# Performance work log

Measured on AMD Instinct MI355X. Metric: run time of the kernel, lower is better.

## Reference

```python
import jax, jax.numpy as jnp
import numpy as np

B, L, R, E, D = 16, 28, 64, 34, 512


def setup_inputs() -> dict:
    key = jax.random.key(0)
    ks = jax.random.split(key, 10)
    logits = jax.random.uniform(ks[0], (B, L, R), dtype=jnp.float32)
    evt_embeddings = jax.random.normal(ks[1], (B, 1, D), dtype=jnp.float32)
    arg_embeddings = jax.random.normal(ks[2], (B, L, D), dtype=jnp.float32)
    # valid-arg counts in [1, L] (used as mask-count multiplier and divisor)
    arg_padding_num = jax.random.randint(ks[3], (B,), 1, L + 1).astype(jnp.float32)
    evt_type_list = jax.random.randint(ks[4], (B,), 0, E)
    s = 1.0 / np.sqrt(D)
    WRT = jax.random.normal(ks[5], (R, D, D), dtype=jnp.float32) * s
    WTT = jax.random.normal(ks[6], (E, D, D), dtype=jnp.float32) * s
    w1 = jax.random.normal(ks[7], (D, 64), dtype=jnp.float32) * s
    b1 = jnp.zeros((64,), dtype=jnp.float32)
    w2 = jax.random.normal(ks[8], (64, 1), dtype=jnp.float32) * (1.0 / 8.0)
    b2 = jnp.zeros((1,), dtype=jnp.float32)
    return {"logits": logits, "evt_embeddings": evt_embeddings,
            "arg_embeddings": arg_embeddings, "arg_padding_num": arg_padding_num,
            "evt_type_list": evt_type_list, "WRT": WRT, "WTT": WTT,
            "w1": w1, "b1": b1, "w2": w2, "b2": b2}


def reference(logits, evt_embeddings, arg_embeddings, arg_padding_num,
              evt_type_list, WRT, WTT, w1, b1, w2, b2):
    # role transition matrix per (event, arg): one-hot/soft select over WRT
    # [B,L,R] x [R,D,D] -> [B,L,D,D]  (dominant, memory-bound intermediate)
    role_mats = jnp.einsum('blr,rde->blde', logits, WRT)
    # event transition matrix: one-hot select over WTT == gather
    evt_mats = WTT[evt_type_list]                      # [B,D,D]
    # event embedding transform: [B,1,D] bmm [B,D,D] -> [B,D]
    evt_trans = jnp.einsum('bd,bde->be', evt_embeddings[:, 0, :], evt_mats)
    # per-arg transform: [B,L,D] bmm [B,L,D,D] -> [B,L,D]
    role_trans = jnp.einsum('bld,blde->ble', arg_embeddings, role_mats)
    # multiply by count, sum over args, divide by count (as in the original)
    role_trans = role_trans * arg_padding_num[:, None, None]
    new_sum = jnp.sum(role_trans, axis=1)              # [B,D]
    div = new_sum / arg_padding_num[:, None]
    graph_embeddings = (div + evt_trans) / 2.0         # [B,D]
    # scorer MLP: Linear(D,64) -> ReLU -> Linear(64,1) -> Sigmoid
    h = jax.nn.relu(graph_embeddings @ w1 + b1)
    score = jax.nn.sigmoid(h @ w2 + b2)                # [B,1]
    return score
```

## Files before the change

kernel.cpp:

```cpp
#include <hip/hip_runtime.h>
#include <math.h>

#define BB 16
#define LL 28
#define RR 64
#define DD 512
#define NROLE 128
#define NEVT  256
#define F4RR  65536

__global__ void __launch_bounds__(256, 2) kernel_a(
    const float* __restrict__ logits,
    const float* __restrict__ arg,
    const float* __restrict__ WRT,
    const float* __restrict__ WTT,
    const float* __restrict__ evt_emb,
    const int*   __restrict__ evt_type,
    float* __restrict__ part,
    float* __restrict__ evt_part)
{
    __shared__ float smem[8192];
    const int t   = threadIdx.x;
    const int bid = blockIdx.x;

    if (bid < NROLE) {
        const int rid = bid;
        const int rp  = rid >> 3;
        const int d0  = (rid & 7) * 64;

        const float4* WBase = (const float4*)(WRT + ((size_t)(4 * rp) * DD + d0) * DD);

        const int e4    = t & 127;
        const int h     = t >> 7;
        const int kbase = 32 * h;

        float4 w[8];
#pragma unroll
        for (int i = 0; i < 8; ++i)
            w[i] = WBase[(size_t)(kbase + i) * 128 + e4];

        {
            const int b  = t >> 4;
            const int d4 = t & 15;
            const float4* ap = (const float4*)(arg) + (size_t)(b * LL) * 128 + (d0 >> 2) + d4;
            const float4* lp = (const float4*)(logits) + (size_t)(b * LL) * 16 + rp;
            float4 g0 = {0.f,0.f,0.f,0.f}, g1 = {0.f,0.f,0.f,0.f};
            float4 g2 = {0.f,0.f,0.f,0.f}, g3 = {0.f,0.f,0.f,0.f};
#pragma unroll 7
            for (int l = 0; l < LL; ++l) {
                const float4 av = ap[(size_t)l * 128];
                const float4 lg = lp[(size_t)l * 16];
                g0.x = fmaf(lg.x, av.x, g0.x); g0.y = fmaf(lg.x, av.y, g0.y);
                g0.z = fmaf(lg.x, av.z, g0.z); g0.w = fmaf(lg.x, av.w, g0.w);
                g1.x = fmaf(lg.y, av.x, g1.x); g1.y = fmaf(lg.y, av.y, g1.y);
                g1.z = fmaf(lg.y, av.z, g1.z); g1.w = fmaf(lg.y, av.w, g1.w);
                g2.x = fmaf(lg.z, av.x, g2.x); g2.y = fmaf(lg.z, av.y, g2.y);
                g2.z = fmaf(lg.z, av.z, g2.z); g2.w = fmaf(lg.z, av.w, g2.w);
                g3.x = fmaf(lg.w, av.x, g3.x); g3.y = fmaf(lg.w, av.y, g3.y);
                g3.z = fmaf(lg.w, av.z, g3.z); g3.w = fmaf(lg.w, av.w, g3.w);
            }
            const int row = 4 * d4;
            smem[       (row + 0) * 16 + b] = g0.x;
            smem[       (row + 1) * 16 + b] = g0.y;
            smem[       (row + 2) * 16 + b] = g0.z;
            smem[       (row + 3) * 16 + b] = g0.w;
            smem[1024 + (row + 0) * 16 + b] = g1.x;
            smem[1024 + (row + 1) * 16 + b] = g1.y;
            smem[1024 + (row + 2) * 16 + b] = g1.z;
            smem[1024 + (row + 3) * 16 + b] = g1.w;
            smem[2048 + (row + 0) * 16 + b] = g2.x;
            smem[2048 + (row + 1) * 16 + b] = g2.y;
            smem[2048 + (row + 2) * 16 + b] = g2.z;
            smem[2048 + (row + 3) * 16 + b] = g2.w;
            smem[3072 + (row + 0) * 16 + b] = g3.x;
            smem[3072 + (row + 1) * 16 + b] = g3.y;
            smem[3072 + (row + 2) * 16 + b] = g3.z;
            smem[3072 + (row + 3) * 16 + b] = g3.w;
        }
        __syncthreads();

        float4 acc[16];
#pragma unroll
        for (int i = 0; i < 16; ++i) acc[i] = make_float4(0.f, 0.f, 0.f, 0.f);

        for (int mb = 0; mb < 16; ++mb) {
            const int mbn = (mb + 1) & 15;
            const size_t nb = (size_t)(mbn >> 2) * F4RR;
            const int kn = kbase + (mbn & 3) * 8;
            float4 wn[8];
#pragma unroll
            for (int i = 0; i < 8; ++i)
                wn[i] = WBase[nb + (size_t)(kn + i) * 128 + e4];

            const float* Gr = smem + (mb >> 2) * 1024;
            const int k0 = kbase + (mb & 3) * 8;
#pragma unroll
            for (int i = 0; i < 8; ++i) {
                const float* gp = Gr + (k0 + i) * 16;
                const float4 ga = ((const float4*)gp)[0];
                const float4 gb = ((const float4*)gp)[1];
                const float4 gc = ((const float4*)gp)[2];
                const float4 gd = ((const float4*)gp)[3];
#define ACC(j, S) \
                acc[j].x = fmaf(S, w[i].x, acc[j].x); \
                acc[j].y = fmaf(S, w[i].y, acc[j].y); \
                acc[j].z = fmaf(S, w[i].z, acc[j].z); \
                acc[j].w = fmaf(S, w[i].w, acc[j].w);
                ACC(0,  ga.x) ACC(1,  ga.y) ACC(2,  ga.z) ACC(3,  ga.w)
                ACC(4,  gb.x) ACC(5,  gb.y) ACC(6,  gb.z) ACC(7,  gb.w)
                ACC(8,  gc.x) ACC(9,  gc.y) ACC(10, gc.z) ACC(11, gc.w)
                ACC(12, gd.x) ACC(13, gd.y) ACC(14, gd.z) ACC(15, gd.w)
#undef ACC
            }
#pragma unroll
            for (int i = 0; i < 8; ++i) w[i] = wn[i];
        }

        __syncthreads();
        float4* cb = (float4*)smem;
        if (h == 1) {
#pragma unroll
            for (int i = 0; i < 16; ++i)
                cb[i * 128 + e4] = acc[i];
        }
        __syncthreads();
        if (h == 0) {
            float4* po = (float4*)part + (size_t)rid * 2048;
#pragma unroll
            for (int i = 0; i < 16; ++i) {
                const float4 v = cb[i * 128 + e4];
                acc[i].x += v.x; acc[i].y += v.y; acc[i].z += v.z; acc[i].w += v.w;
                po[i * 128 + e4] = acc[i];
            }
        }
    } else {
        const int cid = bid - NROLE;
        const int b   = cid >> 4;
        const int dc  = cid & 15;
        const int d0  = dc * 32;
        const int ty  = evt_type[b];
        const float* Wt = WTT + (size_t)ty * DD * DD;
        const int e4 = t & 127;
        const int s  = t >> 7;
        float4 a = {0.f, 0.f, 0.f, 0.f};
#pragma unroll
        for (int db = 0; db < 32; db += 16) {
            float  em[8];
            float4 wv[8];
#pragma unroll
            for (int i = 0; i < 8; ++i) {
                const int d = d0 + db + s + 2 * i;
                em[i] = evt_emb[b * DD + d];
                wv[i] = ((const float4*)(Wt + (size_t)d * DD))[e4];
            }
#pragma unroll
            for (int i = 0; i < 8; ++i) {
                a.x = fmaf(em[i], wv[i].x, a.x);
                a.y = fmaf(em[i], wv[i].y, a.y);
                a.z = fmaf(em[i], wv[i].z, a.z);
                a.w = fmaf(em[i], wv[i].w, a.w);
            }
        }
        float4* sm4 = (float4*)smem;
        if (s == 1) sm4[e4] = a;
        __syncthreads();
        if (s == 0) {
            const float4 q4 = sm4[e4];
            a.x += q4.x; a.y += q4.y; a.z += q4.z; a.w += q4.w;
            ((float4*)evt_part)[(size_t)cid * 128 + e4] = a;
        }
    }
}

__global__ void __launch_bounds__(1024) kernel_tail(
    const float* __restrict__ part,
    const float* __restrict__ evt_part,
    const float* __restrict__ w1,
    const float* __restrict__ b1,
    const float* __restrict__ w2,
    const float* __restrict__ b2,
    float* __restrict__ out)
{
    __shared__ float4 sm4[2048];
    __shared__ float  gsm[512];
    __shared__ float  hred[1024];
    const int b  = blockIdx.x;
    const int t  = threadIdx.x;
    const int e4 = t & 127;
    const int g  = t >> 7;

    const float4* p4  = (const float4*)part;
    const float4* e4p = (const float4*)evt_part;
    float4 s = {0.f, 0.f, 0.f, 0.f};
#pragma unroll
    for (int i = 0; i < 16; ++i) {
        const int rid = g * 16 + i;
        const float4 v = p4[(size_t)rid * 2048 + b * 128 + e4];
        s.x += v.x; s.y += v.y; s.z += v.z; s.w += v.w;
    }
    sm4[g * 128 + e4] = s;
    float4 es = {0.f, 0.f, 0.f, 0.f};
#pragma unroll
    for (int i = 0; i < 2; ++i) {
        const int dc = g * 2 + i;
        const float4 v = e4p[(size_t)(b * 16 + dc) * 128 + e4];
        es.x += v.x; es.y += v.y; es.z += v.z; es.w += v.w;
    }
    sm4[1024 + g * 128 + e4] = es;
    __syncthreads();

    if (t < 128) {
        float4 dv = {0.f,0.f,0.f,0.f}, ev = {0.f,0.f,0.f,0.f};
#pragma unroll
        for (int q = 0; q < 8; ++q) {
            const float4 a = sm4[q * 128 + t];
            const float4 c = sm4[1024 + q * 128 + t];
            dv.x += a.x; dv.y += a.y; dv.z += a.z; dv.w += a.w;
            ev.x += c.x; ev.y += c.y; ev.z += c.z; ev.w += c.w;
        }
        float4 gr;
        gr.x = (dv.x + ev.x) * 0.5f;
        gr.y = (dv.y + ev.y) * 0.5f;
        gr.z = (dv.z + ev.z) * 0.5f;
        gr.w = (dv.w + ev.w) * 0.5f;
        ((float4*)gsm)[t] = gr;
    }
    __syncthreads();

    {
        const int j  = t & 63;
        const int dq = t >> 6;
        float hp = 0.f;
#pragma unroll 8
        for (int i = 0; i < 32; ++i) {
            const int d = dq * 32 + i;
            hp = fmaf(gsm[d], w1[d * 64 + j], hp);
        }
        hred[t] = hp;
    }
    __syncthreads();
    if (t < 64) {
        float hh = b1[t];
#pragma unroll
        for (int q = 0; q < 16; ++q) hh += hred[q * 64 + t];
        hh = fmaxf(hh, 0.f);
        float v = hh * w2[t];
#pragma unroll
        for (int off = 32; off > 0; off >>= 1) v += __shfl_down(v, off, 64);
        if (t == 0) out[b] = 1.f / (1.f + expf(-(v + b2[0])));
    }
}

extern "C" void kernel_launch(void* const* d_in, const int* in_sizes, int n_in,
                              void* d_out, int out_size, void* d_ws, size_t ws_size,
                              hipStream_t stream) {
    const float* logits   = (const float*)d_in[0];
    const float* evt_emb  = (const float*)d_in[1];
    const float* arg_emb  = (const float*)d_in[2];
    const int*   evt_type = (const int*)d_in[4];
    const float* WRT      = (const float*)d_in[5];
    const float* WTT      = (const float*)d_in[6];
    const float* w1       = (const float*)d_in[7];
    const float* b1       = (const float*)d_in[8];
    const float* w2       = (const float*)d_in[9];
    const float* b2       = (const float*)d_in[10];
    float* out = (float*)d_out;

    float* part     = (float*)d_ws;
    float* evt_part = part + (size_t)NROLE * 8192;

    hipLaunchKernelGGL(kernel_a, dim3(NROLE + NEVT), dim3(256), 0, stream,
                       logits, arg_emb, WRT, WTT, evt_emb, evt_type, part, evt_part);
    hipLaunchKernelGGL(kernel_tail, dim3(BB), dim3(1024), 0, stream,
                       part, evt_part, w1, b1, w2, b2, out);
}
```

Baseline: 157.0 us.

## Split role-weight work into 4x more blocks with 2 roles and half-width output each

Each role block now handles 2 roles instead of 4 and half of the output columns, with 4 k-groups of 64 threads instead of 2 groups of 128. This raises the role grid from 128 to 512 blocks so the dominant WRT stream is spread over more CUs. The cost is an extra two-stage shared-memory reduction, recomputing the logits-weighted arg sums in more blocks, and a tail kernel that must sum twice as many partial slices.

```diff
diff --git a/kernel.cpp b/kernel.cpp
--- a/kernel.cpp
+++ b/kernel.cpp
@@ -5,7 +5,7 @@
 #define LL 28
 #define RR 64
 #define DD 512
-#define NROLE 128
+#define NROLE 512
 #define NEVT  256
 #define F4RR  65536
 
@@ -25,39 +25,36 @@
 
     if (bid < NROLE) {
         const int rid = bid;
-        const int rp  = rid >> 3;
-        const int d0  = (rid & 7) * 64;
-
-        const float4* WBase = (const float4*)(WRT + ((size_t)(4 * rp) * DD + d0) * DD);
-
-        const int e4    = t & 127;
-        const int h     = t >> 7;
-        const int kbase = 32 * h;
+        const int rp  = rid >> 4;
+        const int d0  = ((rid >> 1) & 7) * 64;
+        const int eh  = rid & 1;
+
+        const float4* WBase = (const float4*)(WRT + ((size_t)(2 * rp) * DD + d0) * DD);
+
+        const int e4    = t & 63;
+        const int h     = t >> 6;
+        const int co    = eh * 64 + e4;
+        const int kbase = 16 * h;
 
         float4 w[8];
 #pragma unroll
         for (int i = 0; i < 8; ++i)
-            w[i] = WBase[(size_t)(kbase + i) * 128 + e4];
+            w[i] = WBase[(size_t)(kbase + i) * 128 + co];
 
         {
             const int b  = t >> 4;
             const int d4 = t & 15;
             const float4* ap = (const float4*)(arg) + (size_t)(b * LL) * 128 + (d0 >> 2) + d4;
-            const float4* lp = (const float4*)(logits) + (size_t)(b * LL) * 16 + rp;
+            const float2* lp = (const float2*)(logits) + (size_t)(b * LL) * 32 + rp;
             float4 g0 = {0.f,0.f,0.f,0.f}, g1 = {0.f,0.f,0.f,0.f};
-            float4 g2 = {0.f,0.f,0.f,0.f}, g3 = {0.f,0.f,0.f,0.f};
 #pragma unroll 7
             for (int l = 0; l < LL; ++l) {
                 const float4 av = ap[(size_t)l * 128];
-                const float4 lg = lp[(size_t)l * 16];
+                const float2 lg = lp[(size_t)l * 32];
                 g0.x = fmaf(lg.x, av.x, g0.x); g0.y = fmaf(lg.x, av.y, g0.y);
                 g0.z = fmaf(lg.x, av.z, g0.z); g0.w = fmaf(lg.x, av.w, g0.w);
                 g1.x = fmaf(lg.y, av.x, g1.x); g1.y = fmaf(lg.y, av.y, g1.y);
                 g1.z = fmaf(lg.y, av.z, g1.z); g1.w = fmaf(lg.y, av.w, g1.w);
-                g2.x = fmaf(lg.z, av.x, g2.x); g2.y = fmaf(lg.z, av.y, g2.y);
-                g2.z = fmaf(lg.z, av.z, g2.z); g2.w = fmaf(lg.z, av.w, g2.w);
-                g3.x = fmaf(lg.w, av.x, g3.x); g3.y = fmaf(lg.w, av.y, g3.y);
-                g3.z = fmaf(lg.w, av.z, g3.z); g3.w = fmaf(lg.w, av.w, g3.w);
             }
             const int row = 4 * d4;
             smem[       (row + 0) * 16 + b] = g0.x;
@@ -68,14 +65,6 @@
             smem[1024 + (row + 1) * 16 + b] = g1.y;
             smem[1024 + (row + 2) * 16 + b] = g1.z;
             smem[1024 + (row + 3) * 16 + b] = g1.w;
-            smem[2048 + (row + 0) * 16 + b] = g2.x;
-            smem[2048 + (row + 1) * 16 + b] = g2.y;
-            smem[2048 + (row + 2) * 16 + b] = g2.z;
-            smem[2048 + (row + 3) * 16 + b] = g2.w;
-            smem[3072 + (row + 0) * 16 + b] = g3.x;
-            smem[3072 + (row + 1) * 16 + b] = g3.y;
-            smem[3072 + (row + 2) * 16 + b] = g3.z;
-            smem[3072 + (row + 3) * 16 + b] = g3.w;
         }
         __syncthreads();
 
@@ -83,17 +72,17 @@
 #pragma unroll
         for (int i = 0; i < 16; ++i) acc[i] = make_float4(0.f, 0.f, 0.f, 0.f);
 
-        for (int mb = 0; mb < 16; ++mb) {
-            const int mbn = (mb + 1) & 15;
-            const size_t nb = (size_t)(mbn >> 2) * F4RR;
-            const int kn = kbase + (mbn & 3) * 8;
+        for (int mb = 0; mb < 4; ++mb) {
+            const int mbn = (mb + 1) & 3;
+            const size_t nb = (size_t)(mbn >> 1) * F4RR;
+            const int kn = kbase + (mbn & 1) * 8;
             float4 wn[8];
 #pragma unroll
             for (int i = 0; i < 8; ++i)
-                wn[i] = WBase[nb + (size_t)(kn + i) * 128 + e4];
-
-            const float* Gr = smem + (mb >> 2) * 1024;
-            const int k0 = kbase + (mb & 3) * 8;
+                wn[i] = WBase[nb + (size_t)(kn + i) * 128 + co];
+
+            const float* Gr = smem + (mb >> 1) * 1024;
+            const int k0 = kbase + (mb & 1) * 8;
 #pragma unroll
             for (int i = 0; i < 8; ++i) {
                 const float* gp = Gr + (k0 + i) * 16;
@@ -118,19 +107,33 @@
 
         __syncthreads();
         float4* cb = (float4*)smem;
+        if (h >= 2) {
+#pragma unroll
+            for (int i = 0; i < 16; ++i)
+                cb[(h - 2) * 1024 + i * 64 + e4] = acc[i];
+        }
+        __syncthreads();
+        if (h < 2) {
+#pragma unroll
+            for (int i = 0; i < 16; ++i) {
+                const float4 v = cb[h * 1024 + i * 64 + e4];
+                acc[i].x += v.x; acc[i].y += v.y; acc[i].z += v.z; acc[i].w += v.w;
+            }
+        }
+        __syncthreads();
         if (h == 1) {
 #pragma unroll
             for (int i = 0; i < 16; ++i)
-                cb[i * 128 + e4] = acc[i];
+                cb[i * 64 + e4] = acc[i];
         }
         __syncthreads();
         if (h == 0) {
-            float4* po = (float4*)part + (size_t)rid * 2048;
+            float4* po = (float4*)part + (size_t)rid * 1024;
 #pragma unroll
             for (int i = 0; i < 16; ++i) {
-                const float4 v = cb[i * 128 + e4];
+                const float4 v = cb[i * 64 + e4];
                 acc[i].x += v.x; acc[i].y += v.y; acc[i].z += v.z; acc[i].w += v.w;
-                po[i * 128 + e4] = acc[i];
+                po[i * 64 + e4] = acc[i];
             }
         }
     } else {
@@ -188,14 +191,16 @@
     const int t  = threadIdx.x;
     const int e4 = t & 127;
     const int g  = t >> 7;
+    const int eh = e4 >> 6;
+    const int ec = e4 & 63;
 
     const float4* p4  = (const float4*)part;
     const float4* e4p = (const float4*)evt_part;
     float4 s = {0.f, 0.f, 0.f, 0.f};
 #pragma unroll
-    for (int i = 0; i < 16; ++i) {
-        const int rid = g * 16 + i;
-        const float4 v = p4[(size_t)rid * 2048 + b * 128 + e4];
+    for (int i = 0; i < 32; ++i) {
+        const int m = g * 32 + i;
+        const float4 v = p4[(size_t)(2 * m + eh) * 1024 + b * 64 + ec];
         s.x += v.x; s.y += v.y; s.z += v.z; s.w += v.w;
     }
     sm4[g * 128 + e4] = s;
@@ -267,7 +272,7 @@
     float* out = (float*)d_out;
 
     float* part     = (float*)d_ws;
-    float* evt_part = part + (size_t)NROLE * 8192;
+    float* evt_part = part + (size_t)NROLE * 4096;
 
     hipLaunchKernelGGL(kernel_a, dim3(NROLE + NEVT), dim3(256), 0, stream,
                        logits, arg_emb, WRT, WTT, evt_emb, evt_type, part, evt_part);
```

Result: faster. 149.0 us (-5.1%).
